# Kernel optimization log

Measured on AMD Instinct MI355X. Metric: run time of the kernel, lower is better.

Reference implementation:

```python
import jax, jax.numpy as jnp
import numpy as np

D = 1024
H = 16
HD = D // H


def setup_inputs() -> dict:
    key = jax.random.key(0)
    ks = jax.random.split(key, 9)
    s = 1.0 / np.sqrt(D)
    x = jax.random.normal(ks[0], (2, 2048, D), dtype=jnp.float32)
    Wq = jax.random.uniform(ks[1], (D, D), jnp.float32, -s, s)
    bq = jax.random.uniform(ks[2], (D,), jnp.float32, -s, s)
    Wk = jax.random.uniform(ks[3], (D, D), jnp.float32, -s, s)
    bk = jax.random.uniform(ks[4], (D,), jnp.float32, -s, s)
    Wv = jax.random.uniform(ks[5], (D, D), jnp.float32, -s, s)
    bv = jax.random.uniform(ks[6], (D,), jnp.float32, -s, s)
    Wo = jax.random.uniform(ks[7], (D, D), jnp.float32, -s, s)
    bo = jax.random.uniform(ks[8], (D,), jnp.float32, -s, s)
    return {"x": x, "Wq": Wq, "bq": bq, "Wk": Wk, "bk": bk,
            "Wv": Wv, "bv": bv, "Wo": Wo, "bo": bo}


def reference(x, Wq, bq, Wk, bk, Wv, bv, Wo, bo):
    B, S, _ = x.shape
    # project and split heads -> [B, H, S, HD]
    def split(t):
        return t.reshape(B, S, H, HD).transpose(0, 2, 1, 3)
    q = split(x @ Wq + bq)
    k = split(x @ Wk + bk)
    v = split(x @ Wv + bv)
    scores = jnp.einsum('bhqd,bhkd->bhqk', q, k) / np.sqrt(HD).astype(np.float32)
    attn = jax.nn.softmax(scores, axis=-1)
    ctx = jnp.einsum('bhqk,bhkd->bhqd', attn, v)  # [B,H,S,HD]
    ctx = ctx.transpose(0, 2, 1, 3).reshape(B, S, D)
    return ctx @ Wo + bo
```

## Files before the change

kernel.cpp:

```cpp
#include <hip/hip_runtime.h>
#include <hip/hip_bf16.h>
#include <math.h>

#define BB 2
#define SS 2048
#define DD 1024
#define HH 16
#define HD 64
#define MM (BB * SS)

typedef __bf16 bf16;
typedef __attribute__((ext_vector_type(8))) __bf16 bf16x8;
typedef __attribute__((ext_vector_type(4))) __bf16 bf16x4;
typedef __attribute__((ext_vector_type(4))) float f32x4;

#define QSCL 0.18033688011112042f

__device__ __forceinline__ void glds16(const bf16* g, bf16* l) {
    __builtin_amdgcn_global_load_lds(
        (const __attribute__((address_space(1))) void*)g,
        (__attribute__((address_space(3))) void*)l, 16, 0, 0);
}

__global__ __launch_bounds__(256) void cvt_x(const float* __restrict__ x,
                                             bf16* __restrict__ xb) {
    int i = (blockIdx.x * 256 + threadIdx.x) * 4;
    float4 v = *(const float4*)(x + i);
    bf16x4 o;
    o[0] = (bf16)v.x; o[1] = (bf16)v.y; o[2] = (bf16)v.z; o[3] = (bf16)v.w;
    *(bf16x4*)(xb + i) = o;
}

__global__ __launch_bounds__(256) void cvt_w(
    const float* __restrict__ W0, const float* __restrict__ W1,
    const float* __restrict__ W2, const float* __restrict__ W3,
    bf16* __restrict__ Wt) {
    const float* W = (blockIdx.z == 0) ? W0 : (blockIdx.z == 1) ? W1
                   : (blockIdx.z == 2) ? W2 : W3;
    bf16* dst = Wt + (size_t)blockIdx.z * DD * DD;

    __shared__ float T[64][65];
    int k0 = blockIdx.y * 64, n0 = blockIdx.x * 64;
    int tr = threadIdx.x >> 4, tc = (threadIdx.x & 15) * 4;
#pragma unroll
    for (int u = 0; u < 4; u++) {
        int r = tr + u * 16;
        float4 v = *(const float4*)&W[(size_t)(k0 + r) * DD + n0 + tc];
        T[tc + 0][r] = v.x; T[tc + 1][r] = v.y;
        T[tc + 2][r] = v.z; T[tc + 3][r] = v.w;
    }
    __syncthreads();
#pragma unroll
    for (int u = 0; u < 4; u++) {
        int r = tr + u * 16;
        bf16x4 o;
        o[0] = (bf16)T[r][tc + 0]; o[1] = (bf16)T[r][tc + 1];
        o[2] = (bf16)T[r][tc + 2]; o[3] = (bf16)T[r][tc + 3];
        *(bf16x4*)&dst[(size_t)(n0 + r) * DD + k0 + tc] = o;
    }
}

__global__ __launch_bounds__(256) void vt_kernel(const bf16* __restrict__ V,
                                                 bf16* __restrict__ Vt) {
    const int bh = blockIdx.y;
    const int b = bh >> 4, h = bh & 15;
    const int s0 = blockIdx.x * 64;

    __shared__ bf16 T[64][72];
    const int r = threadIdx.x >> 2;
    const int c0 = (threadIdx.x & 3) * 16;

    const bf16* src = V + ((size_t)(b * SS + s0 + r)) * DD + h * HD + c0;
    *(bf16x8*)&T[r][c0]     = *(const bf16x8*)(src);
    *(bf16x8*)&T[r][c0 + 8] = *(const bf16x8*)(src + 8);
    __syncthreads();

    bf16x8 o0, o1;
#pragma unroll
    for (int i = 0; i < 8; i++) o0[i] = T[c0 + i][r];
#pragma unroll
    for (int i = 0; i < 8; i++) o1[i] = T[c0 + 8 + i][r];
    bf16* dst = Vt + ((size_t)bh * HD + r) * SS + s0 + c0;
    *(bf16x8*)dst       = o0;
    *(bf16x8*)(dst + 8) = o1;
}

__global__ __launch_bounds__(256) void mfma_gemm(
    const bf16* __restrict__ A, const bf16* __restrict__ Wt0,
    const float* __restrict__ b0, const float* __restrict__ b1,
    const float* __restrict__ b2,
    bf16* __restrict__ o0, bf16* __restrict__ o1, bf16* __restrict__ o2) {
    const int z = blockIdx.z;
    const bf16* Wt = Wt0 + (size_t)z * DD * DD;
    const float* bias = (z == 0) ? b0 : (z == 1) ? b1 : b2;
    bf16* dstb = (z == 0) ? o0 : (z == 1) ? o1 : o2;
    const float scl = (z == 0) ? QSCL : 1.0f;

    __shared__ __align__(16) bf16 As[128 * 64];
    __shared__ __align__(16) bf16 Bs[128 * 64];

    const int tid = threadIdx.x;
    const int lane = tid & 63;
    const int w = tid >> 6;
    const int l15 = lane & 15, quad = lane >> 4;
    const int m0 = blockIdx.y * 128;
    const int n0 = blockIdx.x * 128;
    const int mw = (w & 1) * 64;
    const int nw = (w >> 1) * 64;

    f32x4 acc[4][4];
#pragma unroll
    for (int i = 0; i < 4; i++)
#pragma unroll
        for (int j = 0; j < 4; j++) acc[i][j] = (f32x4){0.f, 0.f, 0.f, 0.f};

    for (int kt = 0; kt < DD; kt += 64) {
        __syncthreads();
#pragma unroll
        for (int u = 0; u < 4; u++) {
            int j = tid + u * 256;
            int row = j >> 3, cp = j & 7;
            int c = cp ^ (row & 7);
            glds16(A  + (size_t)(m0 + row) * DD + kt + c * 8, &As[j * 8]);
            glds16(Wt + (size_t)(n0 + row) * DD + kt + c * 8, &Bs[j * 8]);
        }
        __syncthreads();

#pragma unroll
        for (int kh = 0; kh < 2; kh++) {
            bf16x8 af[4], bf[4];
#pragma unroll
            for (int i = 0; i < 4; i++) {
                int ra = mw + i * 16 + l15;
                int ja = ra * 8 + ((kh * 4 + quad) ^ (ra & 7));
                af[i] = *(const bf16x8*)&As[ja * 8];
                int rb = nw + i * 16 + l15;
                int jb = rb * 8 + ((kh * 4 + quad) ^ (rb & 7));
                bf[i] = *(const bf16x8*)&Bs[jb * 8];
            }
#pragma unroll
            for (int i = 0; i < 4; i++)
#pragma unroll
                for (int j = 0; j < 4; j++)
                    acc[i][j] = __builtin_amdgcn_mfma_f32_16x16x32_bf16(
                        af[i], bf[j], acc[i][j], 0, 0, 0);
        }
    }

    float bcol[4];
#pragma unroll
    for (int j = 0; j < 4; j++) bcol[j] = bias[n0 + nw + j * 16 + l15];

#pragma unroll
    for (int i = 0; i < 4; i++)
#pragma unroll
        for (int j = 0; j < 4; j++)
#pragma unroll
            for (int r = 0; r < 4; r++) {
                int row = m0 + mw + i * 16 + quad * 4 + r;
                int col = n0 + nw + j * 16 + l15;
                dstb[(size_t)row * DD + col] =
                    (bf16)((acc[i][j][r] + bcol[j]) * scl);
            }
}

__global__ __launch_bounds__(256) void mfma_gemm_out(
    const bf16* __restrict__ A, const bf16* __restrict__ Wt,
    const float* __restrict__ bias, float* __restrict__ out) {
    __shared__ __align__(16) bf16 As[64 * 64];
    __shared__ __align__(16) bf16 Bs[128 * 64];

    const int tid = threadIdx.x;
    const int lane = tid & 63;
    const int w = tid >> 6;
    const int l15 = lane & 15, quad = lane >> 4;
    const int m0 = blockIdx.y * 64;
    const int n0 = blockIdx.x * 128;
    const int mw = (w & 1) * 32;
    const int nw = (w >> 1) * 64;

    f32x4 acc[2][4];
#pragma unroll
    for (int i = 0; i < 2; i++)
#pragma unroll
        for (int j = 0; j < 4; j++) acc[i][j] = (f32x4){0.f, 0.f, 0.f, 0.f};

    for (int kt = 0; kt < DD; kt += 64) {
        __syncthreads();
#pragma unroll
        for (int u = 0; u < 2; u++) {
            int j = tid + u * 256;
            int row = j >> 3, c = (j & 7) ^ (row & 7);
            glds16(A + (size_t)(m0 + row) * DD + kt + c * 8, &As[j * 8]);
        }
#pragma unroll
        for (int u = 0; u < 4; u++) {
            int j = tid + u * 256;
            int row = j >> 3, c = (j & 7) ^ (row & 7);
            glds16(Wt + (size_t)(n0 + row) * DD + kt + c * 8, &Bs[j * 8]);
        }
        __syncthreads();

#pragma unroll
        for (int kh = 0; kh < 2; kh++) {
            bf16x8 af[2], bf[4];
#pragma unroll
            for (int i = 0; i < 2; i++) {
                int ra = mw + i * 16 + l15;
                int ja = ra * 8 + ((kh * 4 + quad) ^ (ra & 7));
                af[i] = *(const bf16x8*)&As[ja * 8];
            }
#pragma unroll
            for (int j = 0; j < 4; j++) {
                int rb = nw + j * 16 + l15;
                int jb = rb * 8 + ((kh * 4 + quad) ^ (rb & 7));
                bf[j] = *(const bf16x8*)&Bs[jb * 8];
            }
#pragma unroll
            for (int i = 0; i < 2; i++)
#pragma unroll
                for (int j = 0; j < 4; j++)
                    acc[i][j] = __builtin_amdgcn_mfma_f32_16x16x32_bf16(
                        af[i], bf[j], acc[i][j], 0, 0, 0);
        }
    }

    float bcol[4];
#pragma unroll
    for (int j = 0; j < 4; j++) bcol[j] = bias[n0 + nw + j * 16 + l15];

#pragma unroll
    for (int i = 0; i < 2; i++)
#pragma unroll
        for (int j = 0; j < 4; j++)
#pragma unroll
            for (int r = 0; r < 4; r++) {
                int row = m0 + mw + i * 16 + quad * 4 + r;
                int col = n0 + nw + j * 16 + l15;
                out[(size_t)row * DD + col] = acc[i][j][r] + bcol[j];
            }
}

__global__ __launch_bounds__(256) void mfma_attn(
    const bf16* __restrict__ Qb, const bf16* __restrict__ Kb,
    const bf16* __restrict__ Vtg, bf16* __restrict__ ctxb) {
    __shared__ __align__(16) bf16 Ks[64 * 64];
    __shared__ __align__(16) bf16 Vs[64 * 64];
    __shared__ __align__(16) bf16 Ps[4][16 * 64];

    const int tid = threadIdx.x;
    const int lane = tid & 63;
    const int w = tid >> 6;
    const int l15 = lane & 15, quad = lane >> 4;
    const int bh = blockIdx.y;
    const int b = bh >> 4, h = bh & 15;
    const int q0 = blockIdx.x * 64;
    const size_t mb = (size_t)b * SS;
    const int hc = h * HD;
    const bf16* Vt_bh = Vtg + (size_t)bh * HD * SS;
    bf16* Pw = &Ps[w][0];

    bf16x8 qf[2];
#pragma unroll
    for (int kh = 0; kh < 2; kh++)
        qf[kh] = *(const bf16x8*)&Qb[(mb + q0 + w * 16 + l15) * DD +
                                     hc + kh * 32 + quad * 8];

    int koff[4][2], voff[4][2], prd[2], pwr[4];
#pragma unroll
    for (int kb = 0; kb < 4; kb++) {
        int rk = kb * 16 + l15;
#pragma unroll
        for (int kh = 0; kh < 2; kh++)
            koff[kb][kh] = (rk * 8 + ((kh * 4 + quad) ^ (rk & 7))) * 8;
    }
#pragma unroll
    for (int nb = 0; nb < 4; nb++) {
        int rv = nb * 16 + l15;
#pragma unroll
        for (int kh = 0; kh < 2; kh++)
            voff[nb][kh] = (rv * 8 + ((kh * 4 + quad) ^ (rv & 7))) * 8;
    }
#pragma unroll
    for (int kh = 0; kh < 2; kh++)
        prd[kh] = l15 * 64 + (((kh * 4 + quad) ^ (l15 & 7)) << 3);
#pragma unroll
    for (int kb = 0; kb < 4; kb++) {
        int cw = kb * 2 + (quad >> 1);
        pwr[kb] = l15 * 64 + ((cw ^ (l15 & 7)) << 3) + (quad & 1) * 4;
    }

    const bf16* gK[2]; const bf16* gV[2];
    bf16 *lK[2], *lV[2];
#pragma unroll
    for (int u = 0; u < 2; u++) {
        int j = tid + u * 256;
        int row = j >> 3, cp = j & 7;
        int c = cp ^ (row & 7);
        gK[u] = Kb + (mb + row) * DD + hc + c * 8;
        gV[u] = Vt_bh + (size_t)row * SS + c * 8;
        lK[u] = &Ks[j * 8];
        lV[u] = &Vs[j * 8];
    }

    float l_cur = 0.0f;
    f32x4 o[4];
#pragma unroll
    for (int nb = 0; nb < 4; nb++) o[nb] = (f32x4){0.f, 0.f, 0.f, 0.f};

    for (int kt = 0; kt < SS; kt += 64) {
        __syncthreads();
#pragma unroll
        for (int u = 0; u < 2; u++) {
            glds16(gK[u], lK[u]);  gK[u] += 64 * DD;
            glds16(gV[u], lV[u]);  gV[u] += 64;
        }
        __syncthreads();

        f32x4 sc[4];
#pragma unroll
        for (int kb = 0; kb < 4; kb++) sc[kb] = (f32x4){0.f, 0.f, 0.f, 0.f};
#pragma unroll
        for (int kb = 0; kb < 4; kb++)
#pragma unroll
            for (int kh = 0; kh < 2; kh++) {
                bf16x8 kf = *(const bf16x8*)&Ks[koff[kb][kh]];
                sc[kb] = __builtin_amdgcn_mfma_f32_16x16x32_bf16(
                    kf, qf[kh], sc[kb], 0, 0, 0);
            }

        float rsum = 0.f;
#pragma unroll
        for (int kb = 0; kb < 4; kb++) {
            bf16x4 pvec;
#pragma unroll
            for (int r = 0; r < 4; r++) {
                float p = exp2f(sc[kb][r]);
                rsum += p;
                pvec[r] = (bf16)p;
            }
            *(bf16x4*)&Pw[pwr[kb]] = pvec;
        }
        rsum += __shfl_xor(rsum, 16, 64);
        rsum += __shfl_xor(rsum, 32, 64);
        l_cur += rsum;

#pragma unroll
        for (int kh = 0; kh < 2; kh++) {
            bf16x8 pf = *(const bf16x8*)&Pw[prd[kh]];
#pragma unroll
            for (int nb = 0; nb < 4; nb++) {
                bf16x8 vf = *(const bf16x8*)&Vs[voff[nb][kh]];
                o[nb] = __builtin_amdgcn_mfma_f32_16x16x32_bf16(
                    pf, vf, o[nb], 0, 0, 0);
            }
        }
    }

    float linv = 1.0f / l_cur;
    float li[4];
#pragma unroll
    for (int r = 0; r < 4; r++) li[r] = __shfl(linv, quad * 4 + r, 64);
#pragma unroll
    for (int nb = 0; nb < 4; nb++)
#pragma unroll
        for (int r = 0; r < 4; r++) {
            int qrow = q0 + w * 16 + quad * 4 + r;
            ctxb[(mb + qrow) * DD + hc + nb * 16 + l15] = (bf16)(o[nb][r] * li[r]);
        }
}

extern "C" void kernel_launch(void* const* d_in, const int* in_sizes, int n_in,
                              void* d_out, int out_size, void* d_ws, size_t ws_size,
                              hipStream_t stream) {
    const float* x  = (const float*)d_in[0];
    const float* Wq = (const float*)d_in[1];
    const float* bq = (const float*)d_in[2];
    const float* Wk = (const float*)d_in[3];
    const float* bk = (const float*)d_in[4];
    const float* Wv = (const float*)d_in[5];
    const float* bv = (const float*)d_in[6];
    const float* Wo = (const float*)d_in[7];
    const float* bo = (const float*)d_in[8];
    float* out = (float*)d_out;

    char* base = (char*)d_ws;
    bf16* xb   = (bf16*)(base);
    bf16* Wt   = (bf16*)(base + (8ull  << 20));
    bf16* Qb   = (bf16*)(base + (16ull << 20));
    bf16* Kb   = (bf16*)(base + (24ull << 20));
    bf16* Vb   = (bf16*)(base + (32ull << 20));
    bf16* ctxb = (bf16*)(base + (40ull << 20));
    bf16* Vtg  = xb;

    cvt_x<<<dim3((MM * DD) / (256 * 4)), dim3(256), 0, stream>>>(x, xb);
    cvt_w<<<dim3(16, 16, 4), dim3(256), 0, stream>>>(Wq, Wk, Wv, Wo, Wt);

    mfma_gemm<<<dim3(DD / 128, MM / 128, 3), dim3(256), 0, stream>>>(
        xb, Wt, bq, bk, bv, Qb, Kb, Vb);

    vt_kernel<<<dim3(SS / 64, BB * HH), dim3(256), 0, stream>>>(Vb, Vtg);

    mfma_attn<<<dim3(SS / 64, BB * HH), dim3(256), 0, stream>>>(Qb, Kb, Vtg, ctxb);

    mfma_gemm_out<<<dim3(DD / 128, MM / 64), dim3(256), 0, stream>>>(
        ctxb, Wt + 3ull * DD * DD, bo, out);
}
```

Baseline: 227.4 us.

## Double-buffer K/V in attention, two query blocks per wave, MFMA row sums

The attention kernel now runs with 128 threads, and each wave handles 32 query rows instead of 16, so every K/V fragment read from LDS feeds two MFMAs. K and V tiles are double-buffered, with the next tile loaded before computing on the current one, and only one barrier per iteration instead of two. Row sums of P come from an MFMA against a ones vector rather than shuffles, and the bf16 packing uses v_cvt_pk_bf16_f32. In exchange the kernel uses more registers and LDS per block and has half as many waves per block, which may reduce latency hiding.

```diff
diff --git a/kernel.cpp b/kernel.cpp
--- a/kernel.cpp
+++ b/kernel.cpp
@@ -20,6 +20,12 @@
     __builtin_amdgcn_global_load_lds(
         (const __attribute__((address_space(1))) void*)g,
         (__attribute__((address_space(3))) void*)l, 16, 0, 0);
+}
+
+__device__ __forceinline__ unsigned cvtpk_bf16(float a, float b) {
+    unsigned r;
+    asm("v_cvt_pk_bf16_f32 %0, %1, %2" : "=v"(r) : "v"(a), "v"(b));
+    return r;
 }
 
 __global__ __launch_bounds__(256) void cvt_x(const float* __restrict__ x,
@@ -241,12 +247,12 @@
             }
 }
 
-__global__ __launch_bounds__(256) void mfma_attn(
+__global__ __launch_bounds__(128) void mfma_attn(
     const bf16* __restrict__ Qb, const bf16* __restrict__ Kb,
     const bf16* __restrict__ Vtg, bf16* __restrict__ ctxb) {
-    __shared__ __align__(16) bf16 Ks[64 * 64];
-    __shared__ __align__(16) bf16 Vs[64 * 64];
-    __shared__ __align__(16) bf16 Ps[4][16 * 64];
+    __shared__ __align__(16) bf16 Ks[2][64 * 64];
+    __shared__ __align__(16) bf16 Vs[2][64 * 64];
+    __shared__ __align__(16) bf16 Ps[2][32 * 64];
 
     const int tid = threadIdx.x;
     const int lane = tid & 63;
@@ -260,11 +266,17 @@
     const bf16* Vt_bh = Vtg + (size_t)bh * HD * SS;
     bf16* Pw = &Ps[w][0];
 
-    bf16x8 qf[2];
-#pragma unroll
-    for (int kh = 0; kh < 2; kh++)
-        qf[kh] = *(const bf16x8*)&Qb[(mb + q0 + w * 16 + l15) * DD +
-                                     hc + kh * 32 + quad * 8];
+    bf16x8 qf[2][2];
+#pragma unroll
+    for (int qb = 0; qb < 2; qb++)
+#pragma unroll
+        for (int kh = 0; kh < 2; kh++)
+            qf[qb][kh] = *(const bf16x8*)&Qb[(mb + q0 + w * 32 + qb * 16 + l15) * DD +
+                                             hc + kh * 32 + quad * 8];
+
+    bf16x8 onev;
+#pragma unroll
+    for (int i = 0; i < 8; i++) onev[i] = (bf16)1.0f;
 
     int koff[4][2], voff[4][2], prd[2], pwr[4];
 #pragma unroll
@@ -290,84 +302,107 @@
         pwr[kb] = l15 * 64 + ((cw ^ (l15 & 7)) << 3) + (quad & 1) * 4;
     }
 
-    const bf16* gK[2]; const bf16* gV[2];
-    bf16 *lK[2], *lV[2];
-#pragma unroll
-    for (int u = 0; u < 2; u++) {
-        int j = tid + u * 256;
+    const bf16* gK[4]; const bf16* gV[4]; int lo_[4];
+#pragma unroll
+    for (int u = 0; u < 4; u++) {
+        int j = tid + u * 128;
         int row = j >> 3, cp = j & 7;
         int c = cp ^ (row & 7);
         gK[u] = Kb + (mb + row) * DD + hc + c * 8;
         gV[u] = Vt_bh + (size_t)row * SS + c * 8;
-        lK[u] = &Ks[j * 8];
-        lV[u] = &Vs[j * 8];
-    }
-
-    float l_cur = 0.0f;
-    f32x4 o[4];
-#pragma unroll
-    for (int nb = 0; nb < 4; nb++) o[nb] = (f32x4){0.f, 0.f, 0.f, 0.f};
-
-    for (int kt = 0; kt < SS; kt += 64) {
+        lo_[u] = j * 8;
+    }
+
+    f32x4 o[2][4], lsum[2];
+#pragma unroll
+    for (int qb = 0; qb < 2; qb++) {
+        lsum[qb] = (f32x4){0.f, 0.f, 0.f, 0.f};
+#pragma unroll
+        for (int nb = 0; nb < 4; nb++) o[qb][nb] = (f32x4){0.f, 0.f, 0.f, 0.f};
+    }
+
+#pragma unroll
+    for (int u = 0; u < 4; u++) {
+        glds16(gK[u], &Ks[0][lo_[u]]);  gK[u] += 64 * DD;
+        glds16(gV[u], &Vs[0][lo_[u]]);  gV[u] += 64;
+    }
+    __syncthreads();
+
+    for (int it = 0; it < SS / 64; ++it) {
+        const int buf = it & 1;
+        if (it + 1 < SS / 64) {
+#pragma unroll
+            for (int u = 0; u < 4; u++) {
+                glds16(gK[u], &Ks[buf ^ 1][lo_[u]]);  gK[u] += 64 * DD;
+                glds16(gV[u], &Vs[buf ^ 1][lo_[u]]);  gV[u] += 64;
+            }
+        }
+
+        f32x4 sc[2][4];
+#pragma unroll
+        for (int qb = 0; qb < 2; qb++)
+#pragma unroll
+            for (int kb = 0; kb < 4; kb++) sc[qb][kb] = (f32x4){0.f, 0.f, 0.f, 0.f};
+#pragma unroll
+        for (int kb = 0; kb < 4; kb++)
+#pragma unroll
+            for (int kh = 0; kh < 2; kh++) {
+                bf16x8 kf = *(const bf16x8*)&Ks[buf][koff[kb][kh]];
+                sc[0][kb] = __builtin_amdgcn_mfma_f32_16x16x32_bf16(
+                    kf, qf[0][kh], sc[0][kb], 0, 0, 0);
+                sc[1][kb] = __builtin_amdgcn_mfma_f32_16x16x32_bf16(
+                    kf, qf[1][kh], sc[1][kb], 0, 0, 0);
+            }
+
+#pragma unroll
+        for (int qb = 0; qb < 2; qb++)
+#pragma unroll
+            for (int kb = 0; kb < 4; kb++) {
+                float p0 = exp2f(sc[qb][kb][0]);
+                float p1 = exp2f(sc[qb][kb][1]);
+                float p2 = exp2f(sc[qb][kb][2]);
+                float p3 = exp2f(sc[qb][kb][3]);
+                uint2 pu;
+                pu.x = cvtpk_bf16(p0, p1);
+                pu.y = cvtpk_bf16(p2, p3);
+                *(uint2*)&Pw[qb * 1024 + pwr[kb]] = pu;
+            }
+
+#pragma unroll
+        for (int kh = 0; kh < 2; kh++) {
+            bf16x8 pf0 = *(const bf16x8*)&Pw[prd[kh]];
+            bf16x8 pf1 = *(const bf16x8*)&Pw[1024 + prd[kh]];
+            lsum[0] = __builtin_amdgcn_mfma_f32_16x16x32_bf16(
+                pf0, onev, lsum[0], 0, 0, 0);
+            lsum[1] = __builtin_amdgcn_mfma_f32_16x16x32_bf16(
+                pf1, onev, lsum[1], 0, 0, 0);
+#pragma unroll
+            for (int nb = 0; nb < 4; nb++) {
+                bf16x8 vf = *(const bf16x8*)&Vs[buf][voff[nb][kh]];
+                o[0][nb] = __builtin_amdgcn_mfma_f32_16x16x32_bf16(
+                    pf0, vf, o[0][nb], 0, 0, 0);
+                o[1][nb] = __builtin_amdgcn_mfma_f32_16x16x32_bf16(
+                    pf1, vf, o[1][nb], 0, 0, 0);
+            }
+        }
+
         __syncthreads();
-#pragma unroll
-        for (int u = 0; u < 2; u++) {
-            glds16(gK[u], lK[u]);  gK[u] += 64 * DD;
-            glds16(gV[u], lV[u]);  gV[u] += 64;
-        }
-        __syncthreads();
-
-        f32x4 sc[4];
-#pragma unroll
-        for (int kb = 0; kb < 4; kb++) sc[kb] = (f32x4){0.f, 0.f, 0.f, 0.f};
-#pragma unroll
-        for (int kb = 0; kb < 4; kb++)
-#pragma unroll
-            for (int kh = 0; kh < 2; kh++) {
-                bf16x8 kf = *(const bf16x8*)&Ks[koff[kb][kh]];
-                sc[kb] = __builtin_amdgcn_mfma_f32_16x16x32_bf16(
-                    kf, qf[kh], sc[kb], 0, 0, 0);
-            }
-
-        float rsum = 0.f;
-#pragma unroll
-        for (int kb = 0; kb < 4; kb++) {
-            bf16x4 pvec;
+    }
+
+#pragma unroll
+    for (int qb = 0; qb < 2; qb++) {
+        float li[4];
+#pragma unroll
+        for (int r = 0; r < 4; r++) li[r] = 1.0f / lsum[qb][r];
+#pragma unroll
+        for (int nb = 0; nb < 4; nb++)
 #pragma unroll
             for (int r = 0; r < 4; r++) {
-                float p = exp2f(sc[kb][r]);
-                rsum += p;
-                pvec[r] = (bf16)p;
-            }
-            *(bf16x4*)&Pw[pwr[kb]] = pvec;
-        }
-        rsum += __shfl_xor(rsum, 16, 64);
-        rsum += __shfl_xor(rsum, 32, 64);
-        l_cur += rsum;
-
-#pragma unroll
-        for (int kh = 0; kh < 2; kh++) {
-            bf16x8 pf = *(const bf16x8*)&Pw[prd[kh]];
-#pragma unroll
-            for (int nb = 0; nb < 4; nb++) {
-                bf16x8 vf = *(const bf16x8*)&Vs[voff[nb][kh]];
-                o[nb] = __builtin_amdgcn_mfma_f32_16x16x32_bf16(
-                    pf, vf, o[nb], 0, 0, 0);
-            }
-        }
-    }
-
-    float linv = 1.0f / l_cur;
-    float li[4];
-#pragma unroll
-    for (int r = 0; r < 4; r++) li[r] = __shfl(linv, quad * 4 + r, 64);
-#pragma unroll
-    for (int nb = 0; nb < 4; nb++)
-#pragma unroll
-        for (int r = 0; r < 4; r++) {
-            int qrow = q0 + w * 16 + quad * 4 + r;
-            ctxb[(mb + qrow) * DD + hc + nb * 16 + l15] = (bf16)(o[nb][r] * li[r]);
-        }
+                int qrow = q0 + w * 32 + qb * 16 + quad * 4 + r;
+                ctxb[(mb + qrow) * DD + hc + nb * 16 + l15] =
+                    (bf16)(o[qb][nb][r] * li[r]);
+            }
+    }
 }
 
 extern "C" void kernel_launch(void* const* d_in, const int* in_sizes, int n_in,
@@ -401,7 +436,7 @@
 
     vt_kernel<<<dim3(SS / 64, BB * HH), dim3(256), 0, stream>>>(Vb, Vtg);
 
-    mfma_attn<<<dim3(SS / 64, BB * HH), dim3(256), 0, stream>>>(Qb, Kb, Vtg, ctxb);
+    mfma_attn<<<dim3(SS / 64, BB * HH), dim3(128), 0, stream>>>(Qb, Kb, Vtg, ctxb);
 
     mfma_gemm_out<<<dim3(DD / 128, MM / 64), dim3(256), 0, stream>>>(
         ctxb, Wt + 3ull * DD * DD, bo, out);
```

Result: slower. 233.0 us (+2.5%).

## Double-buffer K/V tiles and compute softmax row sums via MFMA in attention

Applied to the files above, without the earlier changes.

The attention kernel now double-buffers the K and V shared-memory tiles. It issues the async global-to-LDS loads for the next tile before computing on the current one, so only one barrier per iteration is needed and load latency overlaps with MFMA work. The per-row probability sum is now accumulated by an extra MFMA against a ones vector instead of scalar adds plus cross-lane shuffles. Probabilities are packed to bf16 with v_cvt_pk_bf16_f32 inline asm. In exchange, LDS use for K/V doubles, and the row sum is taken from bf16-rounded probabilities rather than fp32.

```diff
diff --git a/kernel.cpp b/kernel.cpp
--- a/kernel.cpp
+++ b/kernel.cpp
@@ -20,6 +20,12 @@
     __builtin_amdgcn_global_load_lds(
         (const __attribute__((address_space(1))) void*)g,
         (__attribute__((address_space(3))) void*)l, 16, 0, 0);
+}
+
+__device__ __forceinline__ unsigned cvtpk_bf16(float a, float b) {
+    unsigned r;
+    asm("v_cvt_pk_bf16_f32 %0, %1, %2" : "=v"(r) : "v"(a), "v"(b));
+    return r;
 }
 
 __global__ __launch_bounds__(256) void cvt_x(const float* __restrict__ x,
@@ -244,8 +250,8 @@
 __global__ __launch_bounds__(256) void mfma_attn(
     const bf16* __restrict__ Qb, const bf16* __restrict__ Kb,
     const bf16* __restrict__ Vtg, bf16* __restrict__ ctxb) {
-    __shared__ __align__(16) bf16 Ks[64 * 64];
-    __shared__ __align__(16) bf16 Vs[64 * 64];
+    __shared__ __align__(16) bf16 Ks[2][64 * 64];
+    __shared__ __align__(16) bf16 Vs[2][64 * 64];
     __shared__ __align__(16) bf16 Ps[4][16 * 64];
 
     const int tid = threadIdx.x;
@@ -266,6 +272,10 @@
         qf[kh] = *(const bf16x8*)&Qb[(mb + q0 + w * 16 + l15) * DD +
                                      hc + kh * 32 + quad * 8];
 
+    bf16x8 onev;
+#pragma unroll
+    for (int i = 0; i < 8; i++) onev[i] = (bf16)1.0f;
+
     int koff[4][2], voff[4][2], prd[2], pwr[4];
 #pragma unroll
     for (int kb = 0; kb < 4; kb++) {
@@ -290,8 +300,7 @@
         pwr[kb] = l15 * 64 + ((cw ^ (l15 & 7)) << 3) + (quad & 1) * 4;
     }
 
-    const bf16* gK[2]; const bf16* gV[2];
-    bf16 *lK[2], *lV[2];
+    const bf16* gK[2]; const bf16* gV[2]; int lo_[2];
 #pragma unroll
     for (int u = 0; u < 2; u++) {
         int j = tid + u * 256;
@@ -299,23 +308,30 @@
         int c = cp ^ (row & 7);
         gK[u] = Kb + (mb + row) * DD + hc + c * 8;
         gV[u] = Vt_bh + (size_t)row * SS + c * 8;
-        lK[u] = &Ks[j * 8];
-        lV[u] = &Vs[j * 8];
-    }
-
-    float l_cur = 0.0f;
-    f32x4 o[4];
+        lo_[u] = j * 8;
+    }
+
+    f32x4 o[4], lsum;
+    lsum = (f32x4){0.f, 0.f, 0.f, 0.f};
 #pragma unroll
     for (int nb = 0; nb < 4; nb++) o[nb] = (f32x4){0.f, 0.f, 0.f, 0.f};
 
-    for (int kt = 0; kt < SS; kt += 64) {
-        __syncthreads();
-#pragma unroll
-        for (int u = 0; u < 2; u++) {
-            glds16(gK[u], lK[u]);  gK[u] += 64 * DD;
-            glds16(gV[u], lV[u]);  gV[u] += 64;
-        }
-        __syncthreads();
+#pragma unroll
+    for (int u = 0; u < 2; u++) {
+        glds16(gK[u], &Ks[0][lo_[u]]);  gK[u] += 64 * DD;
+        glds16(gV[u], &Vs[0][lo_[u]]);  gV[u] += 64;
+    }
+    __syncthreads();
+
+    for (int it = 0; it < SS / 64; ++it) {
+        const int buf = it & 1;
+        if (it + 1 < SS / 64) {
+#pragma unroll
+            for (int u = 0; u < 2; u++) {
+                glds16(gK[u], &Ks[buf ^ 1][lo_[u]]);  gK[u] += 64 * DD;
+                glds16(gV[u], &Vs[buf ^ 1][lo_[u]]);  gV[u] += 64;
+            }
+        }
 
         f32x4 sc[4];
 #pragma unroll
@@ -324,49 +340,49 @@
         for (int kb = 0; kb < 4; kb++)
 #pragma unroll
             for (int kh = 0; kh < 2; kh++) {
-                bf16x8 kf = *(const bf16x8*)&Ks[koff[kb][kh]];
+                bf16x8 kf = *(const bf16x8*)&Ks[buf][koff[kb][kh]];
                 sc[kb] = __builtin_amdgcn_mfma_f32_16x16x32_bf16(
                     kf, qf[kh], sc[kb], 0, 0, 0);
             }
 
-        float rsum = 0.f;
 #pragma unroll
         for (int kb = 0; kb < 4; kb++) {
-            bf16x4 pvec;
-#pragma unroll
-            for (int r = 0; r < 4; r++) {
-                float p = exp2f(sc[kb][r]);
-                rsum += p;
-                pvec[r] = (bf16)p;
-            }
-            *(bf16x4*)&Pw[pwr[kb]] = pvec;
-        }
-        rsum += __shfl_xor(rsum, 16, 64);
-        rsum += __shfl_xor(rsum, 32, 64);
-        l_cur += rsum;
+            float p0 = exp2f(sc[kb][0]);
+            float p1 = exp2f(sc[kb][1]);
+            float p2 = exp2f(sc[kb][2]);
+            float p3 = exp2f(sc[kb][3]);
+            uint2 pu;
+            pu.x = cvtpk_bf16(p0, p1);
+            pu.y = cvtpk_bf16(p2, p3);
+            *(uint2*)&Pw[pwr[kb]] = pu;
+        }
 
 #pragma unroll
         for (int kh = 0; kh < 2; kh++) {
             bf16x8 pf = *(const bf16x8*)&Pw[prd[kh]];
+            lsum = __builtin_amdgcn_mfma_f32_16x16x32_bf16(
+                pf, onev, lsum, 0, 0, 0);
 #pragma unroll
             for (int nb = 0; nb < 4; nb++) {
-                bf16x8 vf = *(const bf16x8*)&Vs[voff[nb][kh]];
+                bf16x8 vf = *(const bf16x8*)&Vs[buf][voff[nb][kh]];
                 o[nb] = __builtin_amdgcn_mfma_f32_16x16x32_bf16(
                     pf, vf, o[nb], 0, 0, 0);
             }
         }
-    }
-
-    float linv = 1.0f / l_cur;
+
+        __syncthreads();
+    }
+
     float li[4];
 #pragma unroll
-    for (int r = 0; r < 4; r++) li[r] = __shfl(linv, quad * 4 + r, 64);
+    for (int r = 0; r < 4; r++) li[r] = 1.0f / lsum[r];
 #pragma unroll
     for (int nb = 0; nb < 4; nb++)
 #pragma unroll
         for (int r = 0; r < 4; r++) {
             int qrow = q0 + w * 16 + quad * 4 + r;
-            ctxb[(mb + qrow) * DD + hc + nb * 16 + l15] = (bf16)(o[nb][r] * li[r]);
+            ctxb[(mb + qrow) * DD + hc + nb * 16 + l15] =
+                (bf16)(o[nb][r] * li[r]);
         }
 }
 
```

After: 226.3 us. Within noise of the previous version (-0.5%).
